# Kernel optimization log

Measured on AMD Instinct MI355X. Metric: run time of the kernel, lower is better.

## Reference

```python
import jax, jax.numpy as jnp
import numpy as np

HIDDEN = 1024
HEADS = 16
HEAD_DIM = HIDDEN // HEADS


def setup_inputs() -> dict:
    key = jax.random.key(0)
    ks = jax.random.split(key, 12)
    B, S, D = 2, 2048, HIDDEN
    scale = 1.0 / np.sqrt(D)
    return {
        "query": jax.random.normal(ks[0], (B, S, D), jnp.float32),
        "key": jax.random.normal(ks[1], (B, S, D), jnp.float32),
        "value": jax.random.normal(ks[2], (B, S, D), jnp.float32),
        "Wq": jax.random.normal(ks[3], (D, D), jnp.float32) * scale,
        "bq": jnp.zeros((D,), jnp.float32),
        "Wk": jax.random.normal(ks[4], (D, D), jnp.float32) * scale,
        "bk": jnp.zeros((D,), jnp.float32),
        "Wv": jax.random.normal(ks[5], (D, D), jnp.float32) * scale,
        "bv": jnp.zeros((D,), jnp.float32),
        "Wo": jax.random.normal(ks[6], (D, D), jnp.float32) * scale,
        "bo": jnp.zeros((D,), jnp.float32),
    }


def reference(query, key, value, Wq, bq, Wk, bk, Wv, bv, Wo, bo):
    B, S, D = query.shape
    H, Hd = HEADS, HEAD_DIM
    sm_scale = 1.0 / jnp.sqrt(jnp.asarray(Hd, query.dtype))

    def proj(x, W, b):  # nn.Linear: x @ W.T + b, then split heads -> [B,H,S,Hd]
        y = jnp.einsum("bsd,ed->bse", x, W) + b
        return y.reshape(B, S, H, Hd).transpose(0, 2, 1, 3)

    Q = proj(query, Wq, bq)
    K = proj(key, Wk, bk)
    V = proj(value, Wv, bv)

    scores = jnp.einsum("bhqd,bhkd->bhqk", Q, K) * sm_scale  # [B,H,S,S]
    attn = jax.nn.softmax(scores, axis=-1)
    ctx = jnp.einsum("bhqk,bhkd->bhqd", attn, V)
    ctx = ctx.transpose(0, 2, 1, 3).reshape(B, S, D)
    out = jnp.einsum("bsd,ed->bse", ctx, Wo) + bo
    return out
```

## Files before the change

### kernel.cpp

```cpp
#include <hip/hip_runtime.h>
#include <stdint.h>

typedef unsigned short u16;
typedef unsigned int u32;
typedef __attribute__((ext_vector_type(8))) short s16x8;
typedef __attribute__((ext_vector_type(4))) float fx4;

#define AS_GLOBAL __attribute__((address_space(1)))
#define AS_LDS    __attribute__((address_space(3)))

__device__ __forceinline__ void g2l16(const u16* g, u16* l) {
  __builtin_amdgcn_global_load_lds((const AS_GLOBAL unsigned int*)g,
                                   (AS_LDS unsigned int*)l, 16, 0, 0);
}
__device__ __forceinline__ u16 f2bf(float f) {
  u32 u = __float_as_uint(f);
  u += 0x7FFF + ((u >> 16) & 1);
  return (u16)(u >> 16);
}
__device__ __forceinline__ u32 pk2bf(float a, float b) {
  return (u32)f2bf(a) | ((u32)f2bf(b) << 16);
}

__global__ __launch_bounds__(256) void cvt3(const float* __restrict__ a, const float* __restrict__ b,
                                            const float* __restrict__ c, u16* oa, u16* ob, u16* oc, int n4) {
  const float* src = blockIdx.y == 0 ? a : blockIdx.y == 1 ? b : c;
  u16* dst = blockIdx.y == 0 ? oa : blockIdx.y == 1 ? ob : oc;
  int i = blockIdx.x * 256 + threadIdx.x;
  if (i >= n4) return;
  float4 f = ((const float4*)src)[i];
  ushort4 o; o.x = f2bf(f.x); o.y = f2bf(f.y); o.z = f2bf(f.z); o.w = f2bf(f.w);
  ((ushort4*)dst)[i] = o;
}
__global__ __launch_bounds__(256) void cvt4(const float* __restrict__ a, const float* __restrict__ b,
                                            const float* __restrict__ c, const float* __restrict__ d,
                                            u16* oa, u16* ob, u16* oc, u16* od, int n4) {
  const float* src = blockIdx.y == 0 ? a : blockIdx.y == 1 ? b : blockIdx.y == 2 ? c : d;
  u16* dst = blockIdx.y == 0 ? oa : blockIdx.y == 1 ? ob : blockIdx.y == 2 ? oc : od;
  int i = blockIdx.x * 256 + threadIdx.x;
  if (i >= n4) return;
  float4 f = ((const float4*)src)[i];
  ushort4 o; o.x = f2bf(f.x); o.y = f2bf(f.y); o.z = f2bf(f.z); o.w = f2bf(f.w);
  ((ushort4*)dst)[i] = o;
}

__global__ __launch_bounds__(256) void gemm_qkv(
    const u16* __restrict__ Aq, const u16* __restrict__ Ak, const u16* __restrict__ Av,
    const u16* __restrict__ Wq, const u16* __restrict__ Wk, const u16* __restrict__ Wv,
    const float* __restrict__ bq, const float* __restrict__ bk, const float* __restrict__ bv,
    u16* __restrict__ Oq, u16* __restrict__ Ok, u16* __restrict__ Ov)
{
  constexpr int K = 1024;
  __shared__ u16 As[128 * 32];
  __shared__ u16 Bs[128 * 32];
  const int z = blockIdx.z;
  const u16* A = z == 0 ? Aq : z == 1 ? Ak : Av;
  const u16* W = z == 0 ? Wq : z == 1 ? Wk : Wv;
  const float* bias = z == 0 ? bq : z == 1 ? bk : bv;
  u16* outB = z == 0 ? Oq : z == 1 ? Ok : Ov;
  const float scale = z == 0 ? 0.180336880f : 1.0f;

  const int bm = blockIdx.x, bn = blockIdx.y;
  const int tid = threadIdx.x;
  const int lane = tid & 63, wave = tid >> 6;
  const int quad = lane >> 4, col = lane & 15;
  const int wm = wave >> 1, wn = wave & 1;

  const int L0 = tid, L1 = 256 + tid;
  const int r0 = L0 >> 2, c0 = (L0 & 3) ^ ((r0 >> 1) & 3);
  const int r1 = L1 >> 2, c1 = (L1 & 3) ^ ((r1 >> 1) & 3);
  const u16* gA0 = A + (bm * 128 + r0) * K + c0 * 8;
  const u16* gA1 = A + (bm * 128 + r1) * K + c1 * 8;
  const u16* gB0 = W + (bn * 128 + r0) * K + c0 * 8;
  const u16* gB1 = W + (bn * 128 + r1) * K + c1 * 8;
  u16* lA0 = As + L0 * 8; u16* lA1 = As + L1 * 8;
  u16* lB0 = Bs + L0 * 8; u16* lB1 = Bs + L1 * 8;

  const int aRow = wm * 64 + col;
  const int bRow = wn * 64 + col;

  fx4 zero = {0.f, 0.f, 0.f, 0.f};
  fx4 acc[4][4];
#pragma unroll
  for (int i = 0; i < 4; ++i)
#pragma unroll
    for (int j = 0; j < 4; ++j) acc[i][j] = zero;

  for (int kb = 0; kb < K / 32; ++kb) {
    __syncthreads();
    g2l16(gA0 + kb * 32, lA0);
    g2l16(gA1 + kb * 32, lA1);
    g2l16(gB0 + kb * 32, lB0);
    g2l16(gB1 + kb * 32, lB1);
    __syncthreads();
    s16x8 af[4], bf[4];
#pragma unroll
    for (int mt = 0; mt < 4; ++mt) {
      int row = aRow + mt * 16;
      int ch = row * 4 + (quad ^ ((row >> 1) & 3));
      af[mt] = *(const s16x8*)(As + ch * 8);
    }
#pragma unroll
    for (int nt = 0; nt < 4; ++nt) {
      int row = bRow + nt * 16;
      int ch = row * 4 + (quad ^ ((row >> 1) & 3));
      bf[nt] = *(const s16x8*)(Bs + ch * 8);
    }
#pragma unroll
    for (int mt = 0; mt < 4; ++mt)
#pragma unroll
      for (int nt = 0; nt < 4; ++nt)
        acc[mt][nt] = __builtin_amdgcn_mfma_f32_16x16x32_bf16(af[mt], bf[nt], acc[mt][nt], 0, 0, 0);
  }

#pragma unroll
  for (int nt = 0; nt < 4; ++nt) {
    int n = bn * 128 + wn * 64 + nt * 16 + col;
    float bvv = bias[n];
#pragma unroll
    for (int mt = 0; mt < 4; ++mt) {
      int mbase = bm * 128 + wm * 64 + mt * 16 + quad * 4;
#pragma unroll
      for (int reg = 0; reg < 4; ++reg) {
        int m = mbase + reg;
        float v = (acc[mt][nt][reg] + bvv) * scale;
        int b = m >> 11, s = m & 2047;
        int h = n >> 6, hd = n & 63;
        outB[((b * 16 + h) * 2048 + s) * 64 + hd] = f2bf(v);
      }
    }
  }
}

__global__ __launch_bounds__(256) void gemm_out(
    const u16* __restrict__ A, const u16* __restrict__ W,
    const float* __restrict__ bias, float* __restrict__ outF)
{
  constexpr int K = 1024;
  __shared__ u16 As[128 * 32];
  __shared__ u16 Bs[64 * 32];
  const int bm = blockIdx.x, bn = blockIdx.y;
  const int tid = threadIdx.x;
  const int lane = tid & 63, wave = tid >> 6;
  const int quad = lane >> 4, col = lane & 15;
  const int wm = wave >> 1, wn = wave & 1;

  const int L0 = tid, L1 = 256 + tid;
  const int r0 = L0 >> 2, c0 = (L0 & 3) ^ ((r0 >> 1) & 3);
  const int r1 = L1 >> 2, c1 = (L1 & 3) ^ ((r1 >> 1) & 3);
  const u16* gA0 = A + (bm * 128 + r0) * K + c0 * 8;
  const u16* gA1 = A + (bm * 128 + r1) * K + c1 * 8;
  const u16* gB0 = W + (bn * 64 + r0) * K + c0 * 8;
  u16* lA0 = As + L0 * 8; u16* lA1 = As + L1 * 8;
  u16* lB0 = Bs + L0 * 8;

  const int aRow = wm * 64 + col;
  const int bRow = wn * 32 + col;

  fx4 zero = {0.f, 0.f, 0.f, 0.f};
  fx4 acc[4][2];
#pragma unroll
  for (int i = 0; i < 4; ++i)
#pragma unroll
    for (int j = 0; j < 2; ++j) acc[i][j] = zero;

  for (int kb = 0; kb < K / 32; ++kb) {
    __syncthreads();
    g2l16(gA0 + kb * 32, lA0);
    g2l16(gA1 + kb * 32, lA1);
    g2l16(gB0 + kb * 32, lB0);
    __syncthreads();
    s16x8 af[4], bf[2];
#pragma unroll
    for (int mt = 0; mt < 4; ++mt) {
      int row = aRow + mt * 16;
      int ch = row * 4 + (quad ^ ((row >> 1) & 3));
      af[mt] = *(const s16x8*)(As + ch * 8);
    }
#pragma unroll
    for (int nt = 0; nt < 2; ++nt) {
      int row = bRow + nt * 16;
      int ch = row * 4 + (quad ^ ((row >> 1) & 3));
      bf[nt] = *(const s16x8*)(Bs + ch * 8);
    }
#pragma unroll
    for (int mt = 0; mt < 4; ++mt)
#pragma unroll
      for (int nt = 0; nt < 2; ++nt)
        acc[mt][nt] = __builtin_amdgcn_mfma_f32_16x16x32_bf16(af[mt], bf[nt], acc[mt][nt], 0, 0, 0);
  }

#pragma unroll
  for (int nt = 0; nt < 2; ++nt) {
    int n = bn * 64 + wn * 32 + nt * 16 + col;
    float bvv = bias[n];
#pragma unroll
    for (int mt = 0; mt < 4; ++mt) {
      int mbase = bm * 128 + wm * 64 + mt * 16 + quad * 4;
#pragma unroll
      for (int reg = 0; reg < 4; ++reg)
        outF[(mbase + reg) * 1024 + n] = acc[mt][nt][reg] + bvv;
    }
  }
}

__global__ __launch_bounds__(256) void transpose_v(const u16* __restrict__ V,
                                                   u16* __restrict__ Vt) {
  __shared__ u16 tile[64 * 72];
  const int bh = blockIdx.y, s0 = blockIdx.x * 64;
  const int tid = threadIdx.x;
#pragma unroll
  for (int i = 0; i < 2; ++i) {
    int idx = i * 256 + tid;
    int s = idx >> 3, c = idx & 7;
    uint4 v = *(const uint4*)(V + ((size_t)bh * 2048 + s0 + s) * 64 + c * 8);
    const u16* pv = (const u16*)&v;
#pragma unroll
    for (int j = 0; j < 8; ++j) tile[(c * 8 + j) * 72 + s] = pv[j];
  }
  __syncthreads();
#pragma unroll
  for (int i = 0; i < 2; ++i) {
    int idx = i * 256 + tid;
    int d = idx >> 3, c = idx & 7;
    uint4 v = *(const uint4*)(tile + d * 72 + c * 8);
    *(uint4*)(Vt + ((size_t)bh * 64 + d) * 2048 + s0 + c * 8) = v;
  }
}

__global__ __launch_bounds__(256, 4) void flash_attn(
    const u16* __restrict__ Qp, const u16* __restrict__ Kp,
    const u16* __restrict__ Vt, u16* __restrict__ ctx)
{
  __shared__ u16 sh[16384];
  const int qt = blockIdx.x, bh = blockIdx.y;
  const int tid = threadIdx.x, lane = tid & 63, wave = tid >> 6;
  const int quad = lane >> 4, col = lane & 15;
  const int wm = wave >> 1, wn = wave & 1;

  const u16* Qb = Qp + ((size_t)bh * 2048 + qt * 64) * 64;
  const u16* Kb = Kp + (size_t)bh * 2048 * 64;
  const u16* Vb = Vt + (size_t)bh * 64 * 2048;

  s16x8 qf[2][2];
#pragma unroll
  for (int mt = 0; mt < 2; ++mt)
#pragma unroll
    for (int h = 0; h < 2; ++h)
      qf[mt][h] = *(const s16x8*)(Qb + (wm * 32 + mt * 16 + col) * 64 + h * 32 + quad * 8);

  fx4 zero = {0.f, 0.f, 0.f, 0.f};
  fx4 acc_o[2][4], acc_l[2];
#pragma unroll
  for (int mt = 0; mt < 2; ++mt) {
    acc_l[mt] = zero;
#pragma unroll
    for (int dt = 0; dt < 4; ++dt) acc_o[mt][dt] = zero;
  }
  s16x8 ones;
#pragma unroll
  for (int j = 0; j < 8; ++j) ones[j] = (short)0x3F80;

  u16* Vs = sh;
  u16* Pw = sh + 8192 + wave * 2048;

  for (int kv = 0; kv < 16; ++kv) {
    const int n0 = kv * 128;
    __syncthreads();
#pragma unroll
    for (int i = 0; i < 4; ++i) {
      int idx = wave * 256 + i * 64 + lane;
      int d = idx >> 4, c = idx & 15;
      uint4 v = *(const uint4*)(Vb + d * 2048 + n0 + c * 8);
      *(uint4*)(Vs + d * 128 + (c ^ (d & 15)) * 8) = v;
    }
#pragma unroll
    for (int nt = 0; nt < 4; ++nt) {
      const u16* kr = Kb + (n0 + wn * 64 + nt * 16 + col) * 64 + quad * 8;
      s16x8 k0 = *(const s16x8*)(kr);
      s16x8 k1 = *(const s16x8*)(kr + 32);
#pragma unroll
      for (int mt = 0; mt < 2; ++mt) {
        fx4 s = __builtin_amdgcn_mfma_f32_16x16x32_bf16(k0, qf[mt][0], zero, 0, 0, 0);
        s = __builtin_amdgcn_mfma_f32_16x16x32_bf16(k1, qf[mt][1], s, 0, 0, 0);
        int m = mt * 16 + col;
        int cch = 2 * nt + (quad >> 1);
        uint2 w;
        w.x = pk2bf(exp2f(s[0]), exp2f(s[1]));
        w.y = pk2bf(exp2f(s[2]), exp2f(s[3]));
        *(uint2*)(Pw + m * 64 + ((cch ^ (m & 7))) * 8 + (quad & 1) * 4) = w;
      }
    }
    __syncthreads();
#pragma unroll
    for (int ks = 0; ks < 2; ++ks) {
      s16x8 pf[2];
#pragma unroll
      for (int mt = 0; mt < 2; ++mt)
        pf[mt] = *(const s16x8*)(Pw + (mt * 16 + col) * 64 + ((4 * ks + quad) ^ (col & 7)) * 8);
#pragma unroll
      for (int dt = 0; dt < 4; ++dt) {
        s16x8 vf = *(const s16x8*)(Vs + (dt * 16 + col) * 128 + ((wn * 8 + 4 * ks + quad) ^ col) * 8);
#pragma unroll
        for (int mt = 0; mt < 2; ++mt)
          acc_o[mt][dt] = __builtin_amdgcn_mfma_f32_16x16x32_bf16(pf[mt], vf, acc_o[mt][dt], 0, 0, 0);
      }
#pragma unroll
      for (int mt = 0; mt < 2; ++mt)
        acc_l[mt] = __builtin_amdgcn_mfma_f32_16x16x32_bf16(pf[mt], ones, acc_l[mt], 0, 0, 0);
    }
  }

  __syncthreads();
  float* buf = (float*)sh;
  if (wn == 1) {
#pragma unroll
    for (int mt = 0; mt < 2; ++mt) {
#pragma unroll
      for (int dt = 0; dt < 4; ++dt)
#pragma unroll
        for (int e = 0; e < 4; ++e)
          buf[wm * 2560 + ((mt * 4 + dt) * 4 + e) * 64 + lane] = acc_o[mt][dt][e];
#pragma unroll
      for (int e = 0; e < 4; ++e)
        buf[wm * 2560 + (32 + mt * 4 + e) * 64 + lane] = acc_l[mt][e];
    }
  }
  __syncthreads();
  if (wn == 0) {
    const int b = bh >> 4, h = bh & 15;
#pragma unroll
    for (int mt = 0; mt < 2; ++mt) {
      fx4 rl;
#pragma unroll
      for (int e = 0; e < 4; ++e) {
        float l = acc_l[mt][e] + buf[wm * 2560 + (32 + mt * 4 + e) * 64 + lane];
        rl[e] = 1.0f / l;
      }
#pragma unroll
      for (int dt = 0; dt < 4; ++dt)
#pragma unroll
        for (int e = 0; e < 4; ++e) {
          float v = (acc_o[mt][dt][e] + buf[wm * 2560 + ((mt * 4 + dt) * 4 + e) * 64 + lane]) * rl[e];
          int s = qt * 64 + wm * 32 + mt * 16 + quad * 4 + e;
          ctx[((size_t)(b * 2048 + s)) * 1024 + h * 64 + dt * 16 + col] = f2bf(v);
        }
    }
  }
}

extern "C" void kernel_launch(void* const* d_in, const int* in_sizes, int n_in,
                              void* d_out, int out_size, void* d_ws, size_t ws_size,
                              hipStream_t stream) {
  const float* q  = (const float*)d_in[0];
  const float* k  = (const float*)d_in[1];
  const float* v  = (const float*)d_in[2];
  const float* Wq = (const float*)d_in[3];
  const float* bq = (const float*)d_in[4];
  const float* Wk = (const float*)d_in[5];
  const float* bk = (const float*)d_in[6];
  const float* Wv = (const float*)d_in[7];
  const float* bv = (const float*)d_in[8];
  const float* Wo = (const float*)d_in[9];
  const float* bo = (const float*)d_in[10];
  float* out = (float*)d_out;

  char* ws = (char*)d_ws;
  const size_t MB = 1u << 20;
  u16* qb  = (u16*)(ws + 0 * MB);
  u16* kb  = (u16*)(ws + 8 * MB);
  u16* vb  = (u16*)(ws + 16 * MB);
  u16* wqb = (u16*)(ws + 24 * MB);
  u16* wkb = (u16*)(ws + 26 * MB);
  u16* wvb = (u16*)(ws + 28 * MB);
  u16* wob = (u16*)(ws + 30 * MB);
  u16* Qp  = (u16*)(ws + 32 * MB);
  u16* Kp  = (u16*)(ws + 40 * MB);
  u16* Vp  = (u16*)(ws + 48 * MB);
  u16* Vtp = (u16*)(ws + 56 * MB);
  u16* ctx = (u16*)(ws + 64 * MB);

  cvt3<<<dim3(4096, 3), 256, 0, stream>>>(q, k, v, qb, kb, vb, 1048576);
  cvt4<<<dim3(1024, 4), 256, 0, stream>>>(Wq, Wk, Wv, Wo, wqb, wkb, wvb, wob, 262144);

  gemm_qkv<<<dim3(32, 8, 3), 256, 0, stream>>>(qb, kb, vb, wqb, wkb, wvb,
                                               bq, bk, bv, Qp, Kp, Vp);
  transpose_v<<<dim3(32, 32), 256, 0, stream>>>(Vp, Vtp);
  flash_attn<<<dim3(32, 32), 256, 0, stream>>>(Qp, Kp, Vtp, ctx);
  gemm_out<<<dim3(32, 16), 256, 0, stream>>>(ctx, wob, bo, out);
}
```

Baseline: 257.1 us.

## Prefetch K fragments, stage V via direct global-to-LDS loads, tune barriers

```diff
diff --git a/kernel.cpp b/kernel.cpp
--- a/kernel.cpp
+++ b/kernel.cpp
@@ -20,6 +20,11 @@
 }
 __device__ __forceinline__ u32 pk2bf(float a, float b) {
   return (u32)f2bf(a) | ((u32)f2bf(b) << 16);
+}
+__device__ __forceinline__ u32 pkcvt(float a, float b) {
+  u32 r;
+  asm("v_cvt_pk_bf16_f32 %0, %1, %2" : "=v"(r) : "v"(a), "v"(b));
+  return r;
 }
 
 __global__ __launch_bounds__(256) void cvt3(const float* __restrict__ a, const float* __restrict__ b,
@@ -264,34 +269,55 @@
   u16* Vs = sh;
   u16* Pw = sh + 8192 + wave * 2048;
 
+  s16x8 kf0[4], kf1[4];
+  auto loadK = [&](int kvi) {
+#pragma unroll
+    for (int nt = 0; nt < 4; ++nt) {
+      const u16* kr = Kb + (kvi * 128 + wn * 64 + nt * 16 + col) * 64 + quad * 8;
+      kf0[nt] = *(const s16x8*)(kr);
+      kf1[nt] = *(const s16x8*)(kr + 32);
+    }
+  };
+  loadK(0);
+
+  const u16* vsrc[4];
+#pragma unroll
+  for (int i = 0; i < 4; ++i) {
+    int d = wave * 16 + i * 4 + (lane >> 4);
+    int cs = (lane & 15) ^ (d & 15);
+    vsrc[i] = Vb + d * 2048 + cs * 8;
+  }
+
   for (int kv = 0; kv < 16; ++kv) {
     const int n0 = kv * 128;
-    __syncthreads();
-#pragma unroll
-    for (int i = 0; i < 4; ++i) {
-      int idx = wave * 256 + i * 64 + lane;
-      int d = idx >> 4, c = idx & 15;
-      uint4 v = *(const uint4*)(Vb + d * 2048 + n0 + c * 8);
-      *(uint4*)(Vs + d * 128 + (c ^ (d & 15)) * 8) = v;
-    }
+    __builtin_amdgcn_s_barrier();
+#pragma unroll
+    for (int i = 0; i < 4; ++i)
+      g2l16(vsrc[i] + n0, Vs + (wave * 16 + i * 4) * 128);
+
+    __builtin_amdgcn_s_setprio(1);
 #pragma unroll
     for (int nt = 0; nt < 4; ++nt) {
-      const u16* kr = Kb + (n0 + wn * 64 + nt * 16 + col) * 64 + quad * 8;
-      s16x8 k0 = *(const s16x8*)(kr);
-      s16x8 k1 = *(const s16x8*)(kr + 32);
 #pragma unroll
       for (int mt = 0; mt < 2; ++mt) {
-        fx4 s = __builtin_amdgcn_mfma_f32_16x16x32_bf16(k0, qf[mt][0], zero, 0, 0, 0);
-        s = __builtin_amdgcn_mfma_f32_16x16x32_bf16(k1, qf[mt][1], s, 0, 0, 0);
+        fx4 s = __builtin_amdgcn_mfma_f32_16x16x32_bf16(kf0[nt], qf[mt][0], zero, 0, 0, 0);
+        s = __builtin_amdgcn_mfma_f32_16x16x32_bf16(kf1[nt], qf[mt][1], s, 0, 0, 0);
         int m = mt * 16 + col;
         int cch = 2 * nt + (quad >> 1);
         uint2 w;
-        w.x = pk2bf(exp2f(s[0]), exp2f(s[1]));
-        w.y = pk2bf(exp2f(s[2]), exp2f(s[3]));
+        w.x = pkcvt(exp2f(s[0]), exp2f(s[1]));
+        w.y = pkcvt(exp2f(s[2]), exp2f(s[3]));
         *(uint2*)(Pw + m * 64 + ((cch ^ (m & 7))) * 8 + (quad & 1) * 4) = w;
       }
     }
-    __syncthreads();
+    __builtin_amdgcn_s_setprio(0);
+
+    asm volatile("s_waitcnt vmcnt(0)" ::: "memory");
+    loadK((kv + 1) & 15);
+    asm volatile("s_waitcnt lgkmcnt(0)" ::: "memory");
+    __builtin_amdgcn_s_barrier();
+
+    __builtin_amdgcn_s_setprio(1);
 #pragma unroll
     for (int ks = 0; ks < 2; ++ks) {
       s16x8 pf[2];
@@ -309,6 +335,7 @@
       for (int mt = 0; mt < 2; ++mt)
         acc_l[mt] = __builtin_amdgcn_mfma_f32_16x16x32_bf16(pf[mt], ones, acc_l[mt], 0, 0, 0);
     }
+    __builtin_amdgcn_s_setprio(0);
   }
 
   __syncthreads();
```

After: 259.7 us. Within noise of the previous version (+1.0%).
